# Kernel optimization log

Measured on AMD Instinct MI355X. Metric: run time of the kernel, lower is better.

The kernel has to match this reference:

```python
import jax, jax.numpy as jnp
import numpy as np

N = 100000      # nodes
E = 3200000     # edges
NG = 64         # graphs in batch
F_IN, H1, H2 = 128, 128, 64
DENSE = 16 * 8  # first_dense_neurons * second_dense_neurons
LABELS = 2


def setup_inputs() -> dict:
    key = jax.random.key(0)
    ks = jax.random.split(key, 12)
    x = jax.random.normal(ks[0], (N, F_IN), dtype=jnp.float32)
    edge_index = jax.random.randint(ks[1], (2, E), 0, N, dtype=jnp.int32)
    batch = jnp.sort(jax.random.randint(ks[2], (N,), 0, NG, dtype=jnp.int32))
    s = 0.05
    W1 = jax.random.normal(ks[3], (F_IN, H1), dtype=jnp.float32) * s
    b1 = jnp.zeros((H1,), dtype=jnp.float32)
    W2 = jax.random.normal(ks[4], (H1, H2), dtype=jnp.float32) * s
    b2 = jnp.zeros((H2,), dtype=jnp.float32)
    Wf1 = jax.random.normal(ks[5], (H2, DENSE), dtype=jnp.float32) * s
    bf1 = jnp.zeros((DENSE,), dtype=jnp.float32)
    Wf2 = jax.random.normal(ks[6], (DENSE, LABELS), dtype=jnp.float32) * s
    bf2 = jnp.zeros((LABELS,), dtype=jnp.float32)
    return {"x": x, "W1": W1, "b1": b1, "W2": W2, "b2": b2,
            "Wf1": Wf1, "bf1": bf1, "Wf2": Wf2, "bf2": bf2,
            "edge_index": edge_index, "batch": batch}


def _gcn_conv(x, W, b, src, dst, dis):
    # PyG GCNConv: h = x @ W, propagate with sym norm (self-loops included)
    h = x @ W
    coef = (dis[src] * dis[dst])[:, None]          # [E,1]
    agg = jax.ops.segment_sum(h[src] * coef, dst, num_segments=N)
    agg = agg + h * (dis * dis)[:, None]           # self-loop term
    return agg + b


def reference(x, W1, b1, W2, b2, Wf1, bf1, Wf2, bf2, edge_index, batch):
    src, dst = edge_index[0], edge_index[1]
    # degree with self-loops, symmetric normalization D^-1/2 (A+I) D^-1/2
    deg = 1.0 + jax.ops.segment_sum(jnp.ones((E,), x.dtype), dst, num_segments=N)
    dis = jax.lax.rsqrt(deg)
    h1 = jax.nn.relu(_gcn_conv(x, W1, b1, src, dst, dis))
    h2 = jax.nn.relu(_gcn_conv(h1, W2, b2, src, dst, dis))
    a1 = h2 @ Wf1 + bf1                            # [N, DENSE] (dropout: eval mode)
    counts = jax.ops.segment_sum(jnp.ones((N,), x.dtype), batch, num_segments=NG)
    graph_embedding = jax.ops.segment_sum(a1, batch, num_segments=NG) / jnp.maximum(counts, 1.0)[:, None]
    ic_predictions = graph_embedding @ Wf2 + bf2   # [NG, LABELS]
    penalty = jnp.float32(0.0)
    return (graph_embedding, penalty, ic_predictions)
```

## Files before the change

kernel.cpp:

```cpp
#include <hip/hip_runtime.h>


typedef __attribute__((ext_vector_type(8))) short bfrag;
typedef __attribute__((ext_vector_type(16))) float f32x16;
typedef __attribute__((ext_vector_type(2))) float floatx2;

__device__ __forceinline__ unsigned short f2bf(float f) {
    unsigned int u = __builtin_bit_cast(unsigned int, f);
    u = (u + 0x7FFFu + ((u >> 16) & 1u)) >> 16;
    return (unsigned short)u;
}
__device__ __forceinline__ float bf2f(unsigned int lo16) {
    unsigned int v = lo16 << 16;
    return __builtin_bit_cast(float, v);
}
__device__ __forceinline__ unsigned char f2fp8(float f) {
    return (unsigned char)(__builtin_amdgcn_cvt_pk_fp8_f32(f, f, 0, false) & 0xFF);
}
__device__ __forceinline__ void macc8f8(float* acc, const uint2& v, float c) {
    floatx2 f0 = __builtin_amdgcn_cvt_pk_f32_fp8((int)v.x, false);
    floatx2 f1 = __builtin_amdgcn_cvt_pk_f32_fp8((int)v.x, true);
    floatx2 f2 = __builtin_amdgcn_cvt_pk_f32_fp8((int)v.y, false);
    floatx2 f3 = __builtin_amdgcn_cvt_pk_f32_fp8((int)v.y, true);
    acc[0] += f0.x * c; acc[1] += f0.y * c;
    acc[2] += f1.x * c; acc[3] += f1.y * c;
    acc[4] += f2.x * c; acc[5] += f2.y * c;
    acc[6] += f3.x * c; acc[7] += f3.y * c;
}

template <int K, int NC>
__device__ __forceinline__ void wprep_body(int bid, const float* __restrict__ W,
                                           unsigned short* __restrict__ Wf) {
    constexpr int CT = NC / 32, KT = K / 16;
    int idx = bid * 256 + threadIdx.x;
    if (idx >= KT * CT * 64) return;
    int l = idx & 63;
    int fi = idx >> 6;
    int ct = fi % CT, kt = fi / CT;
    int n = ct * 32 + (l & 31);
    int k0 = kt * 16 + 8 * (l >> 5);
    unsigned short v[8];
#pragma unroll
    for (int j = 0; j < 8; ++j) v[j] = f2bf(W[(size_t)(k0 + j) * NC + n]);
    uint4 o;
    o.x = (unsigned)v[0] | ((unsigned)v[1] << 16);
    o.y = (unsigned)v[2] | ((unsigned)v[3] << 16);
    o.z = (unsigned)v[4] | ((unsigned)v[5] << 16);
    o.w = (unsigned)v[6] | ((unsigned)v[7] << 16);
    *(uint4*)&Wf[(size_t)idx * 8] = o;
}

__global__ __launch_bounds__(256) void fusedA_kernel(const int* __restrict__ dst,
                                                     int* __restrict__ bcount, int E, int EB,
                                                     const float* __restrict__ W1,
                                                     unsigned short* __restrict__ Wp1,
                                                     const float* __restrict__ W2,
                                                     unsigned short* __restrict__ Wp2) {
    __shared__ int h[256];
    int b = blockIdx.x;
    int t = threadIdx.x;
    if (b < EB) {
        h[t] = 0;
        __syncthreads();
        int base = b * 4096;
#pragma unroll
        for (int i = 0; i < 16; ++i) {
            int e = base + t + i * 256;
            if (e < E) atomicAdd(&h[dst[e] >> 9], 1);
        }
        __syncthreads();
        if (h[t] > 0) atomicAdd(&bcount[t], h[t]);
    } else if (b < EB + 8) {
        wprep_body<128, 128>(b - EB, W1, Wp1);
    } else {
        wprep_body<128, 64>(b - EB - 8, W2, Wp2);
    }
}

__global__ __launch_bounds__(256) void bucket_scatter_kernel(const int* __restrict__ src,
                                                             const int* __restrict__ dst,
                                                             const int* __restrict__ bcount,
                                                             int* __restrict__ bfill,
                                                             unsigned int* __restrict__ stage,
                                                             int E) {
    __shared__ int sc[256];
    __shared__ int hist[256];
    __shared__ int abase[256];
    int t = threadIdx.x;
    int bc = bcount[t];
    sc[t] = bc;
    __syncthreads();
    for (int off = 1; off < 256; off <<= 1) {
        int tmp = 0;
        if (t >= off) tmp = sc[t - off];
        __syncthreads();
        sc[t] += tmp;
        __syncthreads();
    }
    int bstart_t = sc[t] - bc;
    hist[t] = 0;
    __syncthreads();
    int base = blockIdx.x * 4096;
    int dcache[16];
#pragma unroll
    for (int i = 0; i < 16; ++i) {
        int e = base + t + i * 256;
        dcache[i] = (e < E) ? dst[e] : -1;
        if (dcache[i] >= 0) atomicAdd(&hist[dcache[i] >> 9], 1);
    }
    __syncthreads();
    if (hist[t] > 0) {
        int r = atomicAdd(&bfill[t], hist[t]);
        abase[t] = bstart_t + r;
    }
    __syncthreads();
    hist[t] = 0;
    __syncthreads();
#pragma unroll
    for (int i = 0; i < 16; ++i) {
        int e = base + t + i * 256;
        int d = dcache[i];
        if (d >= 0) {
            int b = d >> 9;
            int slot = atomicAdd(&hist[b], 1);
            stage[abase[b] + slot] = (unsigned)src[e] | ((unsigned)(d & 511) << 17);
        }
    }
}

#define SCAP 14336
__device__ __forceinline__ void csr_build_body(int b, const unsigned int* __restrict__ stage,
                                               const int* __restrict__ bcount,
                                               int* __restrict__ rowstart,
                                               float* __restrict__ dis,
                                               int* __restrict__ csr_src,
                                               int N, int NB, int E) {
    __shared__ int sc[256];
    __shared__ int cnt[512];
    __shared__ int ofs[512];
    __shared__ int psum[256];
    __shared__ unsigned int sedge[SCAP];
    int t = threadIdx.x;
    int bc = bcount[t];
    sc[t] = bc;
    __syncthreads();
    for (int off = 1; off < 256; off <<= 1) {
        int tmp = 0;
        if (t >= off) tmp = sc[t - off];
        __syncthreads();
        sc[t] += tmp;
        __syncthreads();
    }
    int ee = sc[b];
    int eb = ee - bcount[b];
    if (b == NB - 1 && t == 0) rowstart[N] = E;
    int node0 = b << 9;
    int nb = min(512, N - node0);
    cnt[t] = 0;
    cnt[t + 256] = 0;
    __syncthreads();
    for (int e = eb + t; e < ee; e += 256) {
        unsigned w = stage[e];
        int le = e - eb;
        if (le < SCAP) sedge[le] = w;
        atomicAdd(&cnt[w >> 17], 1);
    }
    __syncthreads();
    int a = cnt[2 * t], c = cnt[2 * t + 1];
    int ps = a + c;
    psum[t] = ps;
    __syncthreads();
    for (int off = 1; off < 256; off <<= 1) {
        int tmp = 0;
        if (t >= off) tmp = psum[t - off];
        __syncthreads();
        psum[t] += tmp;
        __syncthreads();
    }
    int ex = psum[t] - ps;
    ofs[2 * t] = ex;
    ofs[2 * t + 1] = ex + a;
    if (2 * t < nb) {
        rowstart[node0 + 2 * t] = eb + ex;
        dis[node0 + 2 * t] = rsqrtf(1.f + (float)a);
    }
    if (2 * t + 1 < nb) {
        rowstart[node0 + 2 * t + 1] = eb + ex + a;
        dis[node0 + 2 * t + 1] = rsqrtf(1.f + (float)c);
    }
    __syncthreads();
    for (int e = eb + t; e < ee; e += 256) {
        int le = e - eb;
        unsigned w = (le < SCAP) ? sedge[le] : stage[e];
        int l = w >> 17;
        int slot = atomicAdd(&ofs[l], 1);
        csr_src[eb + slot] = (int)(w & 0x1FFFFu);
    }
}

template <int K, int NC, bool IN_F32>
__device__ __forceinline__ void gemm_body(int gb, const void* __restrict__ Av,
                                          const unsigned short* __restrict__ Wf,
                                          unsigned char* __restrict__ C, int M) {
    constexpr int KT = K / 16, CT = NC / 32;
    int wid = gb * 4 + (int)(threadIdx.x >> 6);
    int lane = threadIdx.x & 63;
    int row0 = wid * 32;
    if (row0 >= M) return;

    bfrag B[KT][CT];
#pragma unroll
    for (int kt = 0; kt < KT; ++kt)
#pragma unroll
        for (int ct = 0; ct < CT; ++ct)
            B[kt][ct] = *(const bfrag*)&Wf[(size_t)((kt * CT + ct) * 64 + lane) * 8];

    f32x16 acc[CT];
#pragma unroll
    for (int ct = 0; ct < CT; ++ct)
#pragma unroll
        for (int i = 0; i < 16; ++i) acc[ct][i] = 0.f;

    int r = row0 + (lane & 31);
    if (r >= M) r = M - 1;
#pragma unroll
    for (int kt = 0; kt < KT; ++kt) {
        bfrag a;
        if (IN_F32) {
            const float* Arow = &((const float*)Av)[(size_t)r * K + 8 * (lane >> 5)];
            float4 v0 = *(const float4*)&Arow[kt * 16];
            float4 v1 = *(const float4*)&Arow[kt * 16 + 4];
            a[0] = (short)f2bf(v0.x); a[1] = (short)f2bf(v0.y);
            a[2] = (short)f2bf(v0.z); a[3] = (short)f2bf(v0.w);
            a[4] = (short)f2bf(v1.x); a[5] = (short)f2bf(v1.y);
            a[6] = (short)f2bf(v1.z); a[7] = (short)f2bf(v1.w);
        } else {
            const unsigned short* Arow =
                &((const unsigned short*)Av)[(size_t)r * K + 8 * (lane >> 5)];
            a = *(const bfrag*)&Arow[kt * 16];
        }
#pragma unroll
        for (int ct = 0; ct < CT; ++ct)
            acc[ct] = __builtin_amdgcn_mfma_f32_32x32x16_bf16(a, B[kt][ct], acc[ct], 0, 0, 0);
    }

    int colb = lane & 31;
    int rowq = 4 * (lane >> 5);
#pragma unroll
    for (int ct = 0; ct < CT; ++ct) {
        int col = ct * 32 + colb;
#pragma unroll
        for (int rg = 0; rg < 16; ++rg) {
            int row = row0 + (rg & 3) + 8 * (rg >> 2) + rowq;
            if (row < M) C[(size_t)row * NC + col] = f2fp8(acc[ct][rg]);
        }
    }
}

__global__ __launch_bounds__(256) void fusedB_kernel(const unsigned int* __restrict__ stage,
                                                     const int* __restrict__ bcount,
                                                     int* __restrict__ rowstart,
                                                     float* __restrict__ dis,
                                                     int* __restrict__ csr_src,
                                                     int N, int NB, int E,
                                                     const float* __restrict__ x,
                                                     const unsigned short* __restrict__ Wp1,
                                                     unsigned char* __restrict__ hf8) {
    int b = blockIdx.x;
    if (b < NB) {
        csr_build_body(b, stage, bcount, rowstart, dis, csr_src, N, NB, E);
    } else {
        gemm_body<128, 128, true>(b - NB, x, Wp1, hf8, N);
    }
}

template <int K, int NC, bool IN_F32>
__global__ __launch_bounds__(256) void gemm_mfma_kernel(const void* __restrict__ Av,
                                                        const unsigned short* __restrict__ Wf,
                                                        unsigned char* __restrict__ C,
                                                        int M) {
    gemm_body<K, NC, IN_F32>(blockIdx.x, Av, Wf, C, M);
}

template <int NC>
__global__ __launch_bounds__(256) void aggregate_kernel(const unsigned char* __restrict__ h,
                                                        const float* __restrict__ dis,
                                                        const int* __restrict__ rowstart,
                                                        const int* __restrict__ csr_src,
                                                        const float* __restrict__ bias,
                                                        unsigned short* __restrict__ out,
                                                        int N) {
    constexpr int LPR = NC / 8;
    constexpr int RPS = 64 / LPR;
    int wid = (blockIdx.x * blockDim.x + threadIdx.x) >> 6;
    int lane = threadIdx.x & 63;
    if (wid >= N) return;
    int n = wid;
    int sub = lane / LPR;
    int fid = lane % LPR;
    const uint2* h8 = (const uint2*)h;
    float d = dis[n];
    float acc[8];
#pragma unroll
    for (int i = 0; i < 8; ++i) acc[i] = 0.f;
    if (sub == 0) {
        uint2 hv = h8[(size_t)n * LPR + fid];
        macc8f8(acc, hv, d);
    }

    int beg = rowstart[n], end = rowstart[n + 1];
    for (int e0 = beg; e0 < end; e0 += 64) {
        int idx = e0 + lane;
        int sv = 0;
        float dv = 0.f;
        if (idx < end) {
            sv = __builtin_nontemporal_load(&csr_src[idx]);
            dv = dis[sv];
        }
        int cnt = min(64, end - e0);
        int j = 0;
        for (; j + 4 * RPS <= cnt; j += 4 * RPS) {
            int ja = j + sub, jb = j + RPS + sub, jc2 = j + 2 * RPS + sub,
                jd = j + 3 * RPS + sub;
            int sa = __shfl(sv, ja); float ca = __shfl(dv, ja);
            int sb = __shfl(sv, jb); float cb = __shfl(dv, jb);
            int sc = __shfl(sv, jc2); float cc = __shfl(dv, jc2);
            int sd = __shfl(sv, jd); float cd = __shfl(dv, jd);
            uint2 va = h8[(size_t)sa * LPR + fid];
            uint2 vb = h8[(size_t)sb * LPR + fid];
            uint2 vc = h8[(size_t)sc * LPR + fid];
            uint2 vd = h8[(size_t)sd * LPR + fid];
            macc8f8(acc, va, ca);
            macc8f8(acc, vb, cb);
            macc8f8(acc, vc, cc);
            macc8f8(acc, vd, cd);
        }
        for (; j + 2 * RPS <= cnt; j += 2 * RPS) {
            int ja = j + sub, jb = j + RPS + sub;
            int sa = __shfl(sv, ja); float ca = __shfl(dv, ja);
            int sb = __shfl(sv, jb); float cb = __shfl(dv, jb);
            uint2 va = h8[(size_t)sa * LPR + fid];
            uint2 vb = h8[(size_t)sb * LPR + fid];
            macc8f8(acc, va, ca);
            macc8f8(acc, vb, cb);
        }
        for (; j < cnt; j += RPS) {
            int jj = j + sub;
            int jc = min(jj, cnt - 1);
            int s = __shfl(sv, jc);
            float c = __shfl(dv, jc);
            if (jj >= cnt) c = 0.f;
            uint2 v = h8[(size_t)s * LPR + fid];
            macc8f8(acc, v, c);
        }
    }
#pragma unroll
    for (int m = LPR; m < 64; m <<= 1) {
#pragma unroll
        for (int i = 0; i < 8; ++i) acc[i] += __shfl_xor(acc[i], m);
    }
    if (sub == 0) {
        const float4 bv0 = *(const float4*)&bias[fid * 8 + 0];
        const float4 bv1 = *(const float4*)&bias[fid * 8 + 4];
        float r[8];
        r[0] = fmaxf(acc[0] * d + bv0.x, 0.f);
        r[1] = fmaxf(acc[1] * d + bv0.y, 0.f);
        r[2] = fmaxf(acc[2] * d + bv0.z, 0.f);
        r[3] = fmaxf(acc[3] * d + bv0.w, 0.f);
        r[4] = fmaxf(acc[4] * d + bv1.x, 0.f);
        r[5] = fmaxf(acc[5] * d + bv1.y, 0.f);
        r[6] = fmaxf(acc[6] * d + bv1.z, 0.f);
        r[7] = fmaxf(acc[7] * d + bv1.w, 0.f);
        uint4 o;
        o.x = (unsigned)f2bf(r[0]) | ((unsigned)f2bf(r[1]) << 16);
        o.y = (unsigned)f2bf(r[2]) | ((unsigned)f2bf(r[3]) << 16);
        o.z = (unsigned)f2bf(r[4]) | ((unsigned)f2bf(r[5]) << 16);
        o.w = (unsigned)f2bf(r[6]) | ((unsigned)f2bf(r[7]) << 16);
        *(uint4*)&out[(size_t)n * NC + fid * 8] = o;
    }
}

__global__ __launch_bounds__(256) void poolcount_kernel(const unsigned short* __restrict__ h2,
                                                        const int* __restrict__ batch,
                                                        float* __restrict__ gsum,
                                                        int* __restrict__ gcnt,
                                                        int N, int PB) {
    int t = threadIdx.x;
    if ((int)blockIdx.x < PB) {
        int fid = t & 63;
        int strip = t >> 6;
        int n0 = blockIdx.x * 128;
        int nend = min(n0 + 128, N);
        int n = n0 + strip;
        if (n < nend) {
            float acc = 0.f;
            int gcur = batch[n];
            for (; n < nend; n += 4) {
                int g = batch[n];
                if (g != gcur) {
                    atomicAdd(&gsum[gcur * 64 + fid], acc);
                    acc = 0.f;
                    gcur = g;
                }
                acc += bf2f(h2[(size_t)n * 64 + fid]);
            }
            atomicAdd(&gsum[gcur * 64 + fid], acc);
        }
    } else {
        __shared__ int lc[64];
        if (t < 64) lc[t] = 0;
        __syncthreads();
        int n = ((int)blockIdx.x - PB) * 256 + t;
        if (n < N) atomicAdd(&lc[batch[n]], 1);
        __syncthreads();
        if (t < 64 && lc[t] > 0) atomicAdd(&gcnt[t], lc[t]);
    }
}

__global__ __launch_bounds__(128) void head_kernel(const float* __restrict__ gsum,
                                                   const int* __restrict__ gcnt,
                                                   const float* __restrict__ Wf1,
                                                   const float* __restrict__ bf1,
                                                   const float* __restrict__ Wf2,
                                                   const float* __restrict__ bf2,
                                                   float* __restrict__ out) {
    __shared__ float ph[64];
    __shared__ float red0[128], red1[128];
    int g = blockIdx.x, f = threadIdx.x;
    if (f < 64) ph[f] = gsum[g * 64 + f] / (float)max(gcnt[g], 1);
    __syncthreads();
    float ge = bf1[f];
#pragma unroll 8
    for (int k = 0; k < 64; ++k) ge += ph[k] * Wf1[k * 128 + f];
    out[g * 128 + f] = ge;
    red0[f] = ge * Wf2[f * 2 + 0];
    red1[f] = ge * Wf2[f * 2 + 1];
    __syncthreads();
    for (int off = 64; off > 0; off >>= 1) {
        if (f < off) { red0[f] += red0[f + off]; red1[f] += red1[f + off]; }
        __syncthreads();
    }
    if (f == 0) {
        out[8192 + 1 + g * 2 + 0] = red0[0] + bf2[0];
        out[8192 + 1 + g * 2 + 1] = red1[0] + bf2[1];
        if (g == 0) out[8192] = 0.f;
    }
}

extern "C" void kernel_launch(void* const* d_in, const int* in_sizes, int n_in,
                              void* d_out, int out_size, void* d_ws, size_t ws_size,
                              hipStream_t stream) {
    const float* x   = (const float*)d_in[0];
    const float* W1  = (const float*)d_in[1];
    const float* b1  = (const float*)d_in[2];
    const float* W2  = (const float*)d_in[3];
    const float* b2  = (const float*)d_in[4];
    const float* Wf1 = (const float*)d_in[5];
    const float* bf1 = (const float*)d_in[6];
    const float* Wf2 = (const float*)d_in[7];
    const float* bf2 = (const float*)d_in[8];
    const int* edge  = (const int*)d_in[9];
    const int* batch = (const int*)d_in[10];

    const int N = in_sizes[10];
    const int E = in_sizes[9] / 2;
    const int* srcA = edge;
    const int* dstA = edge + E;
    float* out = (float*)d_out;

    const int NB = (N + 511) >> 9;

    char* p = (char*)d_ws;
    auto alloc = [&](size_t bytes) {
        char* r = p;
        p += (bytes + 255) & ~(size_t)255;
        return r;
    };
    float* gsum     = (float*)alloc(64 * 64 * 4);
    int*   gcnt     = (int*)alloc(64 * 4);
    int*   bcount   = (int*)alloc(256 * 4);
    int*   bfill    = (int*)alloc(256 * 4);
    size_t zbytes   = (size_t)(p - (char*)d_ws);
    float* dis      = (float*)alloc((size_t)N * 4);
    int*   rowstart = (int*)alloc((size_t)(N + 1) * 4);
    unsigned short* Wp1 = (unsigned short*)alloc(8 * 4 * 64 * 8 * 2);
    unsigned short* Wp2 = (unsigned short*)alloc(8 * 2 * 64 * 8 * 2);
    unsigned int* stage = (unsigned int*)alloc((size_t)E * 4);
    int*   csr_src  = (int*)alloc((size_t)E * 4);
    unsigned char*  hf8   = (unsigned char*)alloc((size_t)N * 128);
    unsigned short* h1b   = (unsigned short*)alloc((size_t)N * 128 * 2);
    unsigned short* h2b   = (unsigned short*)alloc((size_t)N * 64 * 2);

    (void)hipMemsetAsync(d_ws, 0, zbytes, stream);

    const int EB = (E + 4095) / 4096;
    const int GB = (N + 127) / 128;
    fusedA_kernel<<<EB + 12, 256, 0, stream>>>(dstA, bcount, E, EB, W1, Wp1, W2, Wp2);
    bucket_scatter_kernel<<<EB, 256, 0, stream>>>(srcA, dstA, bcount, bfill, stage, E);
    fusedB_kernel<<<NB + GB, 256, 0, stream>>>(stage, bcount, rowstart, dis, csr_src,
                                               N, NB, E, x, Wp1, hf8);
    aggregate_kernel<128><<<(N + 3) / 4, 256, 0, stream>>>(hf8, dis, rowstart, csr_src,
                                                           b1, h1b, N);
    gemm_mfma_kernel<128, 64, false><<<GB, 256, 0, stream>>>(h1b, Wp2, hf8, N);
    aggregate_kernel<64><<<(N + 3) / 4, 256, 0, stream>>>(hf8, dis, rowstart, csr_src,
                                                          b2, h2b, N);
    const int PB = (N + 127) / 128;
    const int CB = (N + 255) / 256;
    poolcount_kernel<<<PB + CB, 256, 0, stream>>>(h2b, batch, gsum, gcnt, N, PB);
    head_kernel<<<64, 128, 0, stream>>>(gsum, gcnt, Wf1, bf1, Wf2, bf2, out);
}
```

Measured before the change: 380.1 us.

## Fuse layer-1 aggregation with layer-2 GEMM and layer-2 aggregation with pooling

Layer-1 aggregation now writes each 32-node tile of h1 into LDS, and an MFMA GEMM in the same kernel multiplies it by W2 and writes the fp8 layer-2 features. Layer-2 aggregation is fused with mean pooling and graph counting, so the separate GEMM, pool and count kernels and the h1/h2 bf16 round trips to global memory go away. The cost is large 1024-thread blocks where only two waves run the GEMM after a block-wide barrier, and many more global atomics into gsum, since pooling is done per 8-node block.

```diff
diff --git a/kernel.cpp b/kernel.cpp
--- a/kernel.cpp
+++ b/kernel.cpp
@@ -28,286 +28,22 @@
     acc[6] += f3.x * c; acc[7] += f3.y * c;
 }
 
-template <int K, int NC>
-__device__ __forceinline__ void wprep_body(int bid, const float* __restrict__ W,
-                                           unsigned short* __restrict__ Wf) {
-    constexpr int CT = NC / 32, KT = K / 16;
-    int idx = bid * 256 + threadIdx.x;
-    if (idx >= KT * CT * 64) return;
-    int l = idx & 63;
-    int fi = idx >> 6;
-    int ct = fi % CT, kt = fi / CT;
-    int n = ct * 32 + (l & 31);
-    int k0 = kt * 16 + 8 * (l >> 5);
-    unsigned short v[8];
-#pragma unroll
-    for (int j = 0; j < 8; ++j) v[j] = f2bf(W[(size_t)(k0 + j) * NC + n]);
-    uint4 o;
-    o.x = (unsigned)v[0] | ((unsigned)v[1] << 16);
-    o.y = (unsigned)v[2] | ((unsigned)v[3] << 16);
-    o.z = (unsigned)v[4] | ((unsigned)v[5] << 16);
-    o.w = (unsigned)v[6] | ((unsigned)v[7] << 16);
-    *(uint4*)&Wf[(size_t)idx * 8] = o;
-}
-
-__global__ __launch_bounds__(256) void fusedA_kernel(const int* __restrict__ dst,
-                                                     int* __restrict__ bcount, int E, int EB,
-                                                     const float* __restrict__ W1,
-                                                     unsigned short* __restrict__ Wp1,
-                                                     const float* __restrict__ W2,
-                                                     unsigned short* __restrict__ Wp2) {
-    __shared__ int h[256];
-    int b = blockIdx.x;
-    int t = threadIdx.x;
-    if (b < EB) {
-        h[t] = 0;
-        __syncthreads();
-        int base = b * 4096;
-#pragma unroll
-        for (int i = 0; i < 16; ++i) {
-            int e = base + t + i * 256;
-            if (e < E) atomicAdd(&h[dst[e] >> 9], 1);
-        }
-        __syncthreads();
-        if (h[t] > 0) atomicAdd(&bcount[t], h[t]);
-    } else if (b < EB + 8) {
-        wprep_body<128, 128>(b - EB, W1, Wp1);
-    } else {
-        wprep_body<128, 64>(b - EB - 8, W2, Wp2);
-    }
-}
-
-__global__ __launch_bounds__(256) void bucket_scatter_kernel(const int* __restrict__ src,
-                                                             const int* __restrict__ dst,
-                                                             const int* __restrict__ bcount,
-                                                             int* __restrict__ bfill,
-                                                             unsigned int* __restrict__ stage,
-                                                             int E) {
-    __shared__ int sc[256];
-    __shared__ int hist[256];
-    __shared__ int abase[256];
-    int t = threadIdx.x;
-    int bc = bcount[t];
-    sc[t] = bc;
-    __syncthreads();
-    for (int off = 1; off < 256; off <<= 1) {
-        int tmp = 0;
-        if (t >= off) tmp = sc[t - off];
-        __syncthreads();
-        sc[t] += tmp;
-        __syncthreads();
-    }
-    int bstart_t = sc[t] - bc;
-    hist[t] = 0;
-    __syncthreads();
-    int base = blockIdx.x * 4096;
-    int dcache[16];
-#pragma unroll
-    for (int i = 0; i < 16; ++i) {
-        int e = base + t + i * 256;
-        dcache[i] = (e < E) ? dst[e] : -1;
-        if (dcache[i] >= 0) atomicAdd(&hist[dcache[i] >> 9], 1);
-    }
-    __syncthreads();
-    if (hist[t] > 0) {
-        int r = atomicAdd(&bfill[t], hist[t]);
-        abase[t] = bstart_t + r;
-    }
-    __syncthreads();
-    hist[t] = 0;
-    __syncthreads();
-#pragma unroll
-    for (int i = 0; i < 16; ++i) {
-        int e = base + t + i * 256;
-        int d = dcache[i];
-        if (d >= 0) {
-            int b = d >> 9;
-            int slot = atomicAdd(&hist[b], 1);
-            stage[abase[b] + slot] = (unsigned)src[e] | ((unsigned)(d & 511) << 17);
-        }
-    }
-}
-
-#define SCAP 14336
-__device__ __forceinline__ void csr_build_body(int b, const unsigned int* __restrict__ stage,
-                                               const int* __restrict__ bcount,
-                                               int* __restrict__ rowstart,
-                                               float* __restrict__ dis,
-                                               int* __restrict__ csr_src,
-                                               int N, int NB, int E) {
-    __shared__ int sc[256];
-    __shared__ int cnt[512];
-    __shared__ int ofs[512];
-    __shared__ int psum[256];
-    __shared__ unsigned int sedge[SCAP];
-    int t = threadIdx.x;
-    int bc = bcount[t];
-    sc[t] = bc;
-    __syncthreads();
-    for (int off = 1; off < 256; off <<= 1) {
-        int tmp = 0;
-        if (t >= off) tmp = sc[t - off];
-        __syncthreads();
-        sc[t] += tmp;
-        __syncthreads();
-    }
-    int ee = sc[b];
-    int eb = ee - bcount[b];
-    if (b == NB - 1 && t == 0) rowstart[N] = E;
-    int node0 = b << 9;
-    int nb = min(512, N - node0);
-    cnt[t] = 0;
-    cnt[t + 256] = 0;
-    __syncthreads();
-    for (int e = eb + t; e < ee; e += 256) {
-        unsigned w = stage[e];
-        int le = e - eb;
-        if (le < SCAP) sedge[le] = w;
-        atomicAdd(&cnt[w >> 17], 1);
-    }
-    __syncthreads();
-    int a = cnt[2 * t], c = cnt[2 * t + 1];
-    int ps = a + c;
-    psum[t] = ps;
-    __syncthreads();
-    for (int off = 1; off < 256; off <<= 1) {
-        int tmp = 0;
-        if (t >= off) tmp = psum[t - off];
-        __syncthreads();
-        psum[t] += tmp;
-        __syncthreads();
-    }
-    int ex = psum[t] - ps;
-    ofs[2 * t] = ex;
-    ofs[2 * t + 1] = ex + a;
-    if (2 * t < nb) {
-        rowstart[node0 + 2 * t] = eb + ex;
-        dis[node0 + 2 * t] = rsqrtf(1.f + (float)a);
-    }
-    if (2 * t + 1 < nb) {
-        rowstart[node0 + 2 * t + 1] = eb + ex + a;
-        dis[node0 + 2 * t + 1] = rsqrtf(1.f + (float)c);
-    }
-    __syncthreads();
-    for (int e = eb + t; e < ee; e += 256) {
-        int le = e - eb;
-        unsigned w = (le < SCAP) ? sedge[le] : stage[e];
-        int l = w >> 17;
-        int slot = atomicAdd(&ofs[l], 1);
-        csr_src[eb + slot] = (int)(w & 0x1FFFFu);
-    }
-}
-
-template <int K, int NC, bool IN_F32>
-__device__ __forceinline__ void gemm_body(int gb, const void* __restrict__ Av,
-                                          const unsigned short* __restrict__ Wf,
-                                          unsigned char* __restrict__ C, int M) {
-    constexpr int KT = K / 16, CT = NC / 32;
-    int wid = gb * 4 + (int)(threadIdx.x >> 6);
-    int lane = threadIdx.x & 63;
-    int row0 = wid * 32;
-    if (row0 >= M) return;
-
-    bfrag B[KT][CT];
-#pragma unroll
-    for (int kt = 0; kt < KT; ++kt)
-#pragma unroll
-        for (int ct = 0; ct < CT; ++ct)
-            B[kt][ct] = *(const bfrag*)&Wf[(size_t)((kt * CT + ct) * 64 + lane) * 8];
-
-    f32x16 acc[CT];
-#pragma unroll
-    for (int ct = 0; ct < CT; ++ct)
-#pragma unroll
-        for (int i = 0; i < 16; ++i) acc[ct][i] = 0.f;
-
-    int r = row0 + (lane & 31);
-    if (r >= M) r = M - 1;
-#pragma unroll
-    for (int kt = 0; kt < KT; ++kt) {
-        bfrag a;
-        if (IN_F32) {
-            const float* Arow = &((const float*)Av)[(size_t)r * K + 8 * (lane >> 5)];
-            float4 v0 = *(const float4*)&Arow[kt * 16];
-            float4 v1 = *(const float4*)&Arow[kt * 16 + 4];
-            a[0] = (short)f2bf(v0.x); a[1] = (short)f2bf(v0.y);
-            a[2] = (short)f2bf(v0.z); a[3] = (short)f2bf(v0.w);
-            a[4] = (short)f2bf(v1.x); a[5] = (short)f2bf(v1.y);
-            a[6] = (short)f2bf(v1.z); a[7] = (short)f2bf(v1.w);
-        } else {
-            const unsigned short* Arow =
-                &((const unsigned short*)Av)[(size_t)r * K + 8 * (lane >> 5)];
-            a = *(const bfrag*)&Arow[kt * 16];
-        }
-#pragma unroll
-        for (int ct = 0; ct < CT; ++ct)
-            acc[ct] = __builtin_amdgcn_mfma_f32_32x32x16_bf16(a, B[kt][ct], acc[ct], 0, 0, 0);
-    }
-
-    int colb = lane & 31;
-    int rowq = 4 * (lane >> 5);
-#pragma unroll
-    for (int ct = 0; ct < CT; ++ct) {
-        int col = ct * 32 + colb;
-#pragma unroll
-        for (int rg = 0; rg < 16; ++rg) {
-            int row = row0 + (rg & 3) + 8 * (rg >> 2) + rowq;
-            if (row < M) C[(size_t)row * NC + col] = f2fp8(acc[ct][rg]);
-        }
-    }
-}
-
-__global__ __launch_bounds__(256) void fusedB_kernel(const unsigned int* __restrict__ stage,
-                                                     const int* __restrict__ bcount,
-                                                     int* __restrict__ rowstart,
-                                                     float* __restrict__ dis,
-                                                     int* __restrict__ csr_src,
-                                                     int N, int NB, int E,
-                                                     const float* __restrict__ x,
-                                                     const unsigned short* __restrict__ Wp1,
-                                                     unsigned char* __restrict__ hf8) {
-    int b = blockIdx.x;
-    if (b < NB) {
-        csr_build_body(b, stage, bcount, rowstart, dis, csr_src, N, NB, E);
-    } else {
-        gemm_body<128, 128, true>(b - NB, x, Wp1, hf8, N);
-    }
-}
-
-template <int K, int NC, bool IN_F32>
-__global__ __launch_bounds__(256) void gemm_mfma_kernel(const void* __restrict__ Av,
-                                                        const unsigned short* __restrict__ Wf,
-                                                        unsigned char* __restrict__ C,
-                                                        int M) {
-    gemm_body<K, NC, IN_F32>(blockIdx.x, Av, Wf, C, M);
-}
-
 template <int NC>
-__global__ __launch_bounds__(256) void aggregate_kernel(const unsigned char* __restrict__ h,
-                                                        const float* __restrict__ dis,
-                                                        const int* __restrict__ rowstart,
-                                                        const int* __restrict__ csr_src,
-                                                        const float* __restrict__ bias,
-                                                        unsigned short* __restrict__ out,
-                                                        int N) {
+__device__ __forceinline__ void gather_node(const uint2* __restrict__ h8,
+                                            const float* __restrict__ dis,
+                                            const int* __restrict__ rowstart,
+                                            const int* __restrict__ csr_src,
+                                            int n, int lane, float d, float* acc) {
     constexpr int LPR = NC / 8;
     constexpr int RPS = 64 / LPR;
-    int wid = (blockIdx.x * blockDim.x + threadIdx.x) >> 6;
-    int lane = threadIdx.x & 63;
-    if (wid >= N) return;
-    int n = wid;
     int sub = lane / LPR;
     int fid = lane % LPR;
-    const uint2* h8 = (const uint2*)h;
-    float d = dis[n];
-    float acc[8];
 #pragma unroll
     for (int i = 0; i < 8; ++i) acc[i] = 0.f;
     if (sub == 0) {
         uint2 hv = h8[(size_t)n * LPR + fid];
         macc8f8(acc, hv, d);
     }
-
     int beg = rowstart[n], end = rowstart[n + 1];
     for (int e0 = beg; e0 < end; e0 += 64) {
         int idx = e0 + lane;
@@ -359,61 +95,390 @@
 #pragma unroll
         for (int i = 0; i < 8; ++i) acc[i] += __shfl_xor(acc[i], m);
     }
-    if (sub == 0) {
-        const float4 bv0 = *(const float4*)&bias[fid * 8 + 0];
-        const float4 bv1 = *(const float4*)&bias[fid * 8 + 4];
-        float r[8];
-        r[0] = fmaxf(acc[0] * d + bv0.x, 0.f);
-        r[1] = fmaxf(acc[1] * d + bv0.y, 0.f);
-        r[2] = fmaxf(acc[2] * d + bv0.z, 0.f);
-        r[3] = fmaxf(acc[3] * d + bv0.w, 0.f);
-        r[4] = fmaxf(acc[4] * d + bv1.x, 0.f);
-        r[5] = fmaxf(acc[5] * d + bv1.y, 0.f);
-        r[6] = fmaxf(acc[6] * d + bv1.z, 0.f);
-        r[7] = fmaxf(acc[7] * d + bv1.w, 0.f);
-        uint4 o;
-        o.x = (unsigned)f2bf(r[0]) | ((unsigned)f2bf(r[1]) << 16);
-        o.y = (unsigned)f2bf(r[2]) | ((unsigned)f2bf(r[3]) << 16);
-        o.z = (unsigned)f2bf(r[4]) | ((unsigned)f2bf(r[5]) << 16);
-        o.w = (unsigned)f2bf(r[6]) | ((unsigned)f2bf(r[7]) << 16);
-        *(uint4*)&out[(size_t)n * NC + fid * 8] = o;
-    }
-}
-
-__global__ __launch_bounds__(256) void poolcount_kernel(const unsigned short* __restrict__ h2,
-                                                        const int* __restrict__ batch,
-                                                        float* __restrict__ gsum,
-                                                        int* __restrict__ gcnt,
-                                                        int N, int PB) {
+}
+
+template <int K, int NC>
+__device__ __forceinline__ void wprep_body(int bid, const float* __restrict__ W,
+                                           unsigned short* __restrict__ Wf) {
+    constexpr int CT = NC / 32, KT = K / 16;
+    int idx = bid * 256 + threadIdx.x;
+    if (idx >= KT * CT * 64) return;
+    int l = idx & 63;
+    int fi = idx >> 6;
+    int ct = fi % CT, kt = fi / CT;
+    int n = ct * 32 + (l & 31);
+    int k0 = kt * 16 + 8 * (l >> 5);
+    unsigned short v[8];
+#pragma unroll
+    for (int j = 0; j < 8; ++j) v[j] = f2bf(W[(size_t)(k0 + j) * NC + n]);
+    uint4 o;
+    o.x = (unsigned)v[0] | ((unsigned)v[1] << 16);
+    o.y = (unsigned)v[2] | ((unsigned)v[3] << 16);
+    o.z = (unsigned)v[4] | ((unsigned)v[5] << 16);
+    o.w = (unsigned)v[6] | ((unsigned)v[7] << 16);
+    *(uint4*)&Wf[(size_t)idx * 8] = o;
+}
+
+__global__ __launch_bounds__(256) void fusedA_kernel(const int* __restrict__ dst,
+                                                     int* __restrict__ bcount, int E, int EB,
+                                                     const float* __restrict__ W1,
+                                                     unsigned short* __restrict__ Wp1,
+                                                     const float* __restrict__ W2,
+                                                     unsigned short* __restrict__ Wp2) {
+    __shared__ int h[256];
+    int b = blockIdx.x;
     int t = threadIdx.x;
-    if ((int)blockIdx.x < PB) {
-        int fid = t & 63;
-        int strip = t >> 6;
-        int n0 = blockIdx.x * 128;
-        int nend = min(n0 + 128, N);
-        int n = n0 + strip;
-        if (n < nend) {
-            float acc = 0.f;
-            int gcur = batch[n];
-            for (; n < nend; n += 4) {
-                int g = batch[n];
-                if (g != gcur) {
-                    atomicAdd(&gsum[gcur * 64 + fid], acc);
-                    acc = 0.f;
-                    gcur = g;
-                }
-                acc += bf2f(h2[(size_t)n * 64 + fid]);
+    if (b < EB) {
+        h[t] = 0;
+        __syncthreads();
+        int base = b * 4096;
+#pragma unroll
+        for (int i = 0; i < 16; ++i) {
+            int e = base + t + i * 256;
+            if (e < E) atomicAdd(&h[dst[e] >> 9], 1);
+        }
+        __syncthreads();
+        if (h[t] > 0) atomicAdd(&bcount[t], h[t]);
+    } else if (b < EB + 8) {
+        wprep_body<128, 128>(b - EB, W1, Wp1);
+    } else {
+        wprep_body<128, 64>(b - EB - 8, W2, Wp2);
+    }
+}
+
+__global__ __launch_bounds__(256) void bucket_scatter_kernel(const int* __restrict__ src,
+                                                             const int* __restrict__ dst,
+                                                             const int* __restrict__ bcount,
+                                                             int* __restrict__ bfill,
+                                                             unsigned int* __restrict__ stage,
+                                                             int E) {
+    __shared__ int sc[256];
+    __shared__ int hist[256];
+    __shared__ int abase[256];
+    int t = threadIdx.x;
+    int bc = bcount[t];
+    sc[t] = bc;
+    __syncthreads();
+    for (int off = 1; off < 256; off <<= 1) {
+        int tmp = 0;
+        if (t >= off) tmp = sc[t - off];
+        __syncthreads();
+        sc[t] += tmp;
+        __syncthreads();
+    }
+    int bstart_t = sc[t] - bc;
+    hist[t] = 0;
+    __syncthreads();
+    int base = blockIdx.x * 4096;
+    int dcache[16];
+#pragma unroll
+    for (int i = 0; i < 16; ++i) {
+        int e = base + t + i * 256;
+        dcache[i] = (e < E) ? dst[e] : -1;
+        if (dcache[i] >= 0) atomicAdd(&hist[dcache[i] >> 9], 1);
+    }
+    __syncthreads();
+    if (hist[t] > 0) {
+        int r = atomicAdd(&bfill[t], hist[t]);
+        abase[t] = bstart_t + r;
+    }
+    __syncthreads();
+    hist[t] = 0;
+    __syncthreads();
+#pragma unroll
+    for (int i = 0; i < 16; ++i) {
+        int e = base + t + i * 256;
+        int d = dcache[i];
+        if (d >= 0) {
+            int b = d >> 9;
+            int slot = atomicAdd(&hist[b], 1);
+            stage[abase[b] + slot] = (unsigned)src[e] | ((unsigned)(d & 511) << 17);
+        }
+    }
+}
+
+#define SCAP 14336
+__device__ __forceinline__ void csr_build_body(int b, const unsigned int* __restrict__ stage,
+                                               const int* __restrict__ bcount,
+                                               int* __restrict__ rowstart,
+                                               float* __restrict__ dis,
+                                               int* __restrict__ csr_src,
+                                               int N, int NB, int E) {
+    __shared__ int sc[256];
+    __shared__ int cnt[512];
+    __shared__ int ofs[512];
+    __shared__ int psum[256];
+    __shared__ unsigned int sedge[SCAP];
+    int t = threadIdx.x;
+    int bc = bcount[t];
+    sc[t] = bc;
+    __syncthreads();
+    for (int off = 1; off < 256; off <<= 1) {
+        int tmp = 0;
+        if (t >= off) tmp = sc[t - off];
+        __syncthreads();
+        sc[t] += tmp;
+        __syncthreads();
+    }
+    int ee = sc[b];
+    int eb = ee - bcount[b];
+    if (b == NB - 1 && t == 0) rowstart[N] = E;
+    int node0 = b << 9;
+    int nb = min(512, N - node0);
+    cnt[t] = 0;
+    cnt[t + 256] = 0;
+    __syncthreads();
+    for (int e = eb + t; e < ee; e += 256) {
+        unsigned w = stage[e];
+        int le = e - eb;
+        if (le < SCAP) sedge[le] = w;
+        atomicAdd(&cnt[w >> 17], 1);
+    }
+    __syncthreads();
+    int a = cnt[2 * t], c = cnt[2 * t + 1];
+    int ps = a + c;
+    psum[t] = ps;
+    __syncthreads();
+    for (int off = 1; off < 256; off <<= 1) {
+        int tmp = 0;
+        if (t >= off) tmp = psum[t - off];
+        __syncthreads();
+        psum[t] += tmp;
+        __syncthreads();
+    }
+    int ex = psum[t] - ps;
+    ofs[2 * t] = ex;
+    ofs[2 * t + 1] = ex + a;
+    if (2 * t < nb) {
+        rowstart[node0 + 2 * t] = eb + ex;
+        dis[node0 + 2 * t] = rsqrtf(1.f + (float)a);
+    }
+    if (2 * t + 1 < nb) {
+        rowstart[node0 + 2 * t + 1] = eb + ex + a;
+        dis[node0 + 2 * t + 1] = rsqrtf(1.f + (float)c);
+    }
+    __syncthreads();
+    for (int e = eb + t; e < ee; e += 256) {
+        int le = e - eb;
+        unsigned w = (le < SCAP) ? sedge[le] : stage[e];
+        int l = w >> 17;
+        int slot = atomicAdd(&ofs[l], 1);
+        csr_src[eb + slot] = (int)(w & 0x1FFFFu);
+    }
+}
+
+template <int K, int NC, bool IN_F32>
+__device__ __forceinline__ void gemm_body(int gb, const void* __restrict__ Av,
+                                          const unsigned short* __restrict__ Wf,
+                                          unsigned char* __restrict__ C, int M) {
+    constexpr int KT = K / 16, CT = NC / 32;
+    int wid = gb * 4 + (int)(threadIdx.x >> 6);
+    int lane = threadIdx.x & 63;
+    int row0 = wid * 32;
+    if (row0 >= M) return;
+
+    bfrag B[KT][CT];
+#pragma unroll
+    for (int kt = 0; kt < KT; ++kt)
+#pragma unroll
+        for (int ct = 0; ct < CT; ++ct)
+            B[kt][ct] = *(const bfrag*)&Wf[(size_t)((kt * CT + ct) * 64 + lane) * 8];
+
+    f32x16 acc[CT];
+#pragma unroll
+    for (int ct = 0; ct < CT; ++ct)
+#pragma unroll
+        for (int i = 0; i < 16; ++i) acc[ct][i] = 0.f;
+
+    int r = row0 + (lane & 31);
+    if (r >= M) r = M - 1;
+#pragma unroll
+    for (int kt = 0; kt < KT; ++kt) {
+        bfrag a;
+        if (IN_F32) {
+            const float* Arow = &((const float*)Av)[(size_t)r * K + 8 * (lane >> 5)];
+            float4 v0 = *(const float4*)&Arow[kt * 16];
+            float4 v1 = *(const float4*)&Arow[kt * 16 + 4];
+            a[0] = (short)f2bf(v0.x); a[1] = (short)f2bf(v0.y);
+            a[2] = (short)f2bf(v0.z); a[3] = (short)f2bf(v0.w);
+            a[4] = (short)f2bf(v1.x); a[5] = (short)f2bf(v1.y);
+            a[6] = (short)f2bf(v1.z); a[7] = (short)f2bf(v1.w);
+        } else {
+            const unsigned short* Arow =
+                &((const unsigned short*)Av)[(size_t)r * K + 8 * (lane >> 5)];
+            a = *(const bfrag*)&Arow[kt * 16];
+        }
+#pragma unroll
+        for (int ct = 0; ct < CT; ++ct)
+            acc[ct] = __builtin_amdgcn_mfma_f32_32x32x16_bf16(a, B[kt][ct], acc[ct], 0, 0, 0);
+    }
+
+    int colb = lane & 31;
+    int rowq = 4 * (lane >> 5);
+#pragma unroll
+    for (int ct = 0; ct < CT; ++ct) {
+        int col = ct * 32 + colb;
+#pragma unroll
+        for (int rg = 0; rg < 16; ++rg) {
+            int row = row0 + (rg & 3) + 8 * (rg >> 2) + rowq;
+            if (row < M) C[(size_t)row * NC + col] = f2fp8(acc[ct][rg]);
+        }
+    }
+}
+
+__global__ __launch_bounds__(256) void fusedB_kernel(const unsigned int* __restrict__ stage,
+                                                     const int* __restrict__ bcount,
+                                                     int* __restrict__ rowstart,
+                                                     float* __restrict__ dis,
+                                                     int* __restrict__ csr_src,
+                                                     int N, int NB, int E,
+                                                     const float* __restrict__ x,
+                                                     const unsigned short* __restrict__ Wp1,
+                                                     unsigned char* __restrict__ hf8) {
+    int b = blockIdx.x;
+    if (b < NB) {
+        csr_build_body(b, stage, bcount, rowstart, dis, csr_src, N, NB, E);
+    } else {
+        gemm_body<128, 128, true>(b - NB, x, Wp1, hf8, N);
+    }
+}
+
+__global__ __launch_bounds__(1024) void agg128g_kernel(const unsigned char* __restrict__ h,
+                                                       const float* __restrict__ dis,
+                                                       const int* __restrict__ rowstart,
+                                                       const int* __restrict__ csr_src,
+                                                       const float* __restrict__ bias,
+                                                       const unsigned short* __restrict__ Wp2,
+                                                       unsigned char* __restrict__ gf8,
+                                                       int N) {
+    __shared__ unsigned short lds_h1[32 * 128];
+    int w = threadIdx.x >> 6;
+    int lane = threadIdx.x & 63;
+    int node0 = blockIdx.x * 32;
+    const uint2* h8 = (const uint2*)h;
+    int fid = lane & 15;
+    int sub = lane >> 4;
+#pragma unroll 1
+    for (int j = 0; j < 2; ++j) {
+        int lrow = w * 2 + j;
+        int n = node0 + lrow;
+        if (n < N) {
+            float d = dis[n];
+            float acc[8];
+            gather_node<128>(h8, dis, rowstart, csr_src, n, lane, d, acc);
+            if (sub == 0) {
+                const float4 bv0 = *(const float4*)&bias[fid * 8 + 0];
+                const float4 bv1 = *(const float4*)&bias[fid * 8 + 4];
+                float r[8];
+                r[0] = fmaxf(acc[0] * d + bv0.x, 0.f);
+                r[1] = fmaxf(acc[1] * d + bv0.y, 0.f);
+                r[2] = fmaxf(acc[2] * d + bv0.z, 0.f);
+                r[3] = fmaxf(acc[3] * d + bv0.w, 0.f);
+                r[4] = fmaxf(acc[4] * d + bv1.x, 0.f);
+                r[5] = fmaxf(acc[5] * d + bv1.y, 0.f);
+                r[6] = fmaxf(acc[6] * d + bv1.z, 0.f);
+                r[7] = fmaxf(acc[7] * d + bv1.w, 0.f);
+                uint4 o;
+                o.x = (unsigned)f2bf(r[0]) | ((unsigned)f2bf(r[1]) << 16);
+                o.y = (unsigned)f2bf(r[2]) | ((unsigned)f2bf(r[3]) << 16);
+                o.z = (unsigned)f2bf(r[4]) | ((unsigned)f2bf(r[5]) << 16);
+                o.w = (unsigned)f2bf(r[6]) | ((unsigned)f2bf(r[7]) << 16);
+                *(uint4*)&lds_h1[lrow * 128 + fid * 8] = o;
             }
-            atomicAdd(&gsum[gcur * 64 + fid], acc);
-        }
-    } else {
-        __shared__ int lc[64];
-        if (t < 64) lc[t] = 0;
-        __syncthreads();
-        int n = ((int)blockIdx.x - PB) * 256 + t;
-        if (n < N) atomicAdd(&lc[batch[n]], 1);
-        __syncthreads();
-        if (t < 64 && lc[t] > 0) atomicAdd(&gcnt[t], lc[t]);
+        } else if (sub == 0) {
+            uint4 z = make_uint4(0, 0, 0, 0);
+            *(uint4*)&lds_h1[lrow * 128 + fid * 8] = z;
+        }
+    }
+    __syncthreads();
+    if (w < 2) {
+        int ct = w;
+        f32x16 acc;
+#pragma unroll
+        for (int i = 0; i < 16; ++i) acc[i] = 0.f;
+#pragma unroll 1
+        for (int kt = 0; kt < 8; ++kt) {
+            bfrag a = *(const bfrag*)&lds_h1[(lane & 31) * 128 + kt * 16 + 8 * (lane >> 5)];
+            bfrag Bf = *(const bfrag*)&Wp2[(size_t)((kt * 2 + ct) * 64 + lane) * 8];
+            acc = __builtin_amdgcn_mfma_f32_32x32x16_bf16(a, Bf, acc, 0, 0, 0);
+        }
+        int colb = lane & 31;
+        int rowq = 4 * (lane >> 5);
+        int col = ct * 32 + colb;
+#pragma unroll
+        for (int rg = 0; rg < 16; ++rg) {
+            int lrow = (rg & 3) + 8 * (rg >> 2) + rowq;
+            int node = node0 + lrow;
+            if (node < N) gf8[(size_t)node * 64 + col] = f2fp8(acc[rg]);
+        }
+    }
+}
+
+__global__ __launch_bounds__(512) void agg64p_kernel(const unsigned char* __restrict__ g,
+                                                     const float* __restrict__ dis,
+                                                     const int* __restrict__ rowstart,
+                                                     const int* __restrict__ csr_src,
+                                                     const float* __restrict__ bias,
+                                                     const int* __restrict__ batch,
+                                                     float* __restrict__ gsum,
+                                                     int* __restrict__ gcnt,
+                                                     int N) {
+    __shared__ float tile[8][64];
+    __shared__ int sb[8];
+    int w = threadIdx.x >> 6;
+    int lane = threadIdx.x & 63;
+    int n = blockIdx.x * 8 + w;
+    const uint2* h8 = (const uint2*)g;
+    int fid = lane & 7;
+    int sub = lane >> 3;
+    if (threadIdx.x < 8) {
+        int nn = blockIdx.x * 8 + (int)threadIdx.x;
+        sb[threadIdx.x] = (nn < N) ? batch[nn] : -1;
+    }
+    if (n < N) {
+        float d = dis[n];
+        float acc[8];
+        gather_node<64>(h8, dis, rowstart, csr_src, n, lane, d, acc);
+        if (sub == 0) {
+            const float4 bv0 = *(const float4*)&bias[fid * 8 + 0];
+            const float4 bv1 = *(const float4*)&bias[fid * 8 + 4];
+            float r[8];
+            r[0] = fmaxf(acc[0] * d + bv0.x, 0.f);
+            r[1] = fmaxf(acc[1] * d + bv0.y, 0.f);
+            r[2] = fmaxf(acc[2] * d + bv0.z, 0.f);
+            r[3] = fmaxf(acc[3] * d + bv0.w, 0.f);
+            r[4] = fmaxf(acc[4] * d + bv1.x, 0.f);
+            r[5] = fmaxf(acc[5] * d + bv1.y, 0.f);
+            r[6] = fmaxf(acc[6] * d + bv1.z, 0.f);
+            r[7] = fmaxf(acc[7] * d + bv1.w, 0.f);
+#pragma unroll
+            for (int i = 0; i < 8; ++i)
+                tile[w][fid * 8 + i] = bf2f(f2bf(r[i]));
+        }
+    } else if (sub == 0) {
+#pragma unroll
+        for (int i = 0; i < 8; ++i) tile[w][fid * 8 + i] = 0.f;
+    }
+    __syncthreads();
+    int t = threadIdx.x;
+    if (t < 64) {
+        float a = 0.f;
+        int gcur = -1;
+#pragma unroll
+        for (int r2 = 0; r2 < 8; ++r2) {
+            int g2 = sb[r2];
+            if (g2 < 0) continue;
+            if (g2 != gcur) {
+                if (gcur >= 0) atomicAdd(&gsum[gcur * 64 + t], a);
+                a = 0.f;
+                gcur = g2;
+            }
+            a += tile[r2][t];
+        }
+        if (gcur >= 0) atomicAdd(&gsum[gcur * 64 + t], a);
+    } else if (t < 72) {
+        int r2 = t - 64;
+        if (sb[r2] >= 0) atomicAdd(&gcnt[sb[r2]], 1);
     }
 }
 
@@ -487,9 +552,8 @@
     unsigned short* Wp2 = (unsigned short*)alloc(8 * 2 * 64 * 8 * 2);
     unsigned int* stage = (unsigned int*)alloc((size_t)E * 4);
     int*   csr_src  = (int*)alloc((size_t)E * 4);
-    unsigned char*  hf8   = (unsigned char*)alloc((size_t)N * 128);
-    unsigned short* h1b   = (unsigned short*)alloc((size_t)N * 128 * 2);
-    unsigned short* h2b   = (unsigned short*)alloc((size_t)N * 64 * 2);
+    unsigned char* hf8  = (unsigned char*)alloc((size_t)N * 128);
+    unsigned char* gf8  = (unsigned char*)alloc((size_t)N * 64);
 
     (void)hipMemsetAsync(d_ws, 0, zbytes, stream);
 
@@ -499,13 +563,9 @@
     bucket_scatter_kernel<<<EB, 256, 0, stream>>>(srcA, dstA, bcount, bfill, stage, E);
     fusedB_kernel<<<NB + GB, 256, 0, stream>>>(stage, bcount, rowstart, dis, csr_src,
                                                N, NB, E, x, Wp1, hf8);
-    aggregate_kernel<128><<<(N + 3) / 4, 256, 0, stream>>>(hf8, dis, rowstart, csr_src,
-                                                           b1, h1b, N);
-    gemm_mfma_kernel<128, 64, false><<<GB, 256, 0, stream>>>(h1b, Wp2, hf8, N);
-    aggregate_kernel<64><<<(N + 3) / 4, 256, 0, stream>>>(hf8, dis, rowstart, csr_src,
-                                                          b2, h2b, N);
-    const int PB = (N + 127) / 128;
-    const int CB = (N + 255) / 256;
-    poolcount_kernel<<<PB + CB, 256, 0, stream>>>(h2b, batch, gsum, gcnt, N, PB);
+    agg128g_kernel<<<(N + 31) / 32, 1024, 0, stream>>>(hf8, dis, rowstart, csr_src,
+                                                       b1, Wp2, gf8, N);
+    agg64p_kernel<<<(N + 7) / 8, 512, 0, stream>>>(gf8, dis, rowstart, csr_src,
+                                                   b2, batch, gsum, gcnt, N);
     head_kernel<<<64, 128, 0, stream>>>(gsum, gcnt, Wf1, bf1, Wf2, bf2, out);
 }
```

New measurement: 1.130 ms. 2.97x slower.
